# Kernel optimization log

Measured on AMD Instinct MI355X. Metric: run time of the kernel, lower is better.

The kernel has to match this reference:

```python
import jax, jax.numpy as jnp
import numpy as np

B, S, E, P = 4, 2048, 1024, 4096

def setup_inputs() -> dict:
    key = jax.random.key(0)
    kx, kk, kv = jax.random.split(key, 3)
    x = jax.random.normal(kx, (B, S, E), dtype=jnp.float32)
    K = jax.random.normal(kk, (P, E), dtype=jnp.float32)
    V = jax.random.normal(kv, (P, E), dtype=jnp.float32)
    return {"x": x, "K": K, "V": V}

def reference(x, K, V):
    # scores: [B, S, P] = x @ K^T scaled by 1/sqrt(E)
    scale = jnp.asarray(x.shape[-1], x.dtype) ** -0.5
    scores = jnp.einsum('bse,pe->bsp', x, K) * scale
    attn = jax.nn.softmax(scores, axis=-1)
    # output: [B, S, E] = attn @ V
    return jnp.einsum('bsp,pe->bse', attn, V)
```

## Files before the change

kernel.cpp:

```cpp
#include <hip/hip_runtime.h>
#include <hip/hip_bf16.h>

typedef __attribute__((ext_vector_type(8))) short bf16x8;
typedef __attribute__((ext_vector_type(4))) float f32x4;
typedef __attribute__((ext_vector_type(8))) unsigned short u16x8;

__device__ __forceinline__ unsigned short f2bf(float f) {
  union { float f; unsigned u; } c; c.f = f;
  unsigned u = c.u;
  u = (u + 0x7FFFu + ((u >> 16) & 1u)) >> 16;
  return (unsigned short)u;
}

__device__ __forceinline__ void gld_lds16(const void* g, void* l) {
  __builtin_amdgcn_global_load_lds(
      (__attribute__((address_space(1))) unsigned int*)g,
      (__attribute__((address_space(3))) unsigned int*)l,
      16, 0, 0);
}

__global__ void cvt_all(const float* __restrict__ x, unsigned short* __restrict__ x16,
                        const float* __restrict__ Kw, unsigned short* __restrict__ K16,
                        const float* __restrict__ V, unsigned short* __restrict__ Vt,
                        float* __restrict__ lsum) {
  const int b = blockIdx.x;
  if (b < 32) lsum[b * 256 + threadIdx.x] = 0.f;

  if (b < 6144) {
    const float* in;
    unsigned short* out;
    int i;
    if (b < 4096) {
      in = x; out = x16; i = (b * 256 + threadIdx.x) * 8;
    } else {
      in = Kw; out = K16; i = ((b - 4096) * 256 + threadIdx.x) * 8;
    }
    const float4* p = (const float4*)(in + i);
    float4 a = p[0], bb = p[1];
    u16x8 r;
    r[0] = f2bf(a.x); r[1] = f2bf(a.y); r[2] = f2bf(a.z); r[3] = f2bf(a.w);
    r[4] = f2bf(bb.x); r[5] = f2bf(bb.y); r[6] = f2bf(bb.z); r[7] = f2bf(bb.w);
    *(u16x8*)(out + i) = r;
  } else {
    __shared__ unsigned short t[64][65];
    const int tile = b - 6144;
    const int p0 = (tile & 63) * 64;
    const int e0 = (tile >> 6) * 64;
    const int tx = threadIdx.x & 63;
    const int ty = threadIdx.x >> 6;
#pragma unroll
    for (int i = 0; i < 16; ++i) {
      int p = ty + i * 4;
      t[p][tx] = f2bf(V[(size_t)(p0 + p) * 1024 + e0 + tx]);
    }
    __syncthreads();
#pragma unroll
    for (int i = 0; i < 16; ++i) {
      int e = ty + i * 4;
      Vt[(size_t)(e0 + e) * 4096 + p0 + tx] = t[tx][e];
    }
  }
}

template <int EPI>
__global__ __launch_bounds__(256) void gemm_nt(
    const unsigned short* __restrict__ A, const unsigned short* __restrict__ B,
    int M, int N, int Kd,
    unsigned short* __restrict__ Pout, float* __restrict__ lsum,
    float* __restrict__ Cout, const float* __restrict__ lin, float scale) {
  __shared__ __align__(16) unsigned short sA[128 * 64];
  __shared__ __align__(16) unsigned short sB[128 * 64];

  const int tid = threadIdx.x;
  const int lane = tid & 63;
  const int w = tid >> 6;
  const int wm = w >> 1;
  const int wn = w & 1;

  int row0, col0;
  if constexpr (EPI == 0) {
    row0 = blockIdx.y * 128;
    col0 = blockIdx.x * 128;
  } else {
    int bid = blockIdx.x;
    row0 = (((bid >> 6) << 3) | (bid & 7)) * 128;
    col0 = ((bid >> 3) & 7) * 128;
  }

  f32x4 acc[4][4] = {};

  const unsigned short* pA[4];
  const unsigned short* pB[4];
  char* ldsA[4];
  char* ldsB[4];
#pragma unroll
  for (int j = 0; j < 4; ++j) {
    int c = j * 256 + tid;
    int r = c >> 3;
    int cs = (c & 7) ^ (r & 7);
    pA[j] = A + (size_t)(row0 + r) * Kd + cs * 8;
    pB[j] = B + (size_t)(col0 + r) * Kd + cs * 8;
    int off = (j * 256 + (w << 6)) * 16;
    ldsA[j] = (char*)sA + off;
    ldsB[j] = (char*)sB + off;
  }

  const int q = lane >> 4;
  const int ml = lane & 15;
  const char* fA[2];
  const char* fB[2];
#pragma unroll
  for (int ks = 0; ks < 2; ++ks) {
    int cc = (ks * 4 + q) ^ (ml & 7);
    fA[ks] = (const char*)sA + (wm * 64 + ml) * 128 + cc * 16;
    fB[ks] = (const char*)sB + (wn * 64 + ml) * 128 + cc * 16;
  }

  const int kIters = Kd >> 6;
  for (int it = 0; it < kIters; ++it) {
    __syncthreads();
#pragma unroll
    for (int j = 0; j < 4; ++j) {
      gld_lds16(pA[j], ldsA[j]);
      gld_lds16(pB[j], ldsB[j]);
      pA[j] += 64;
      pB[j] += 64;
    }
    __syncthreads();

#pragma unroll
    for (int ks = 0; ks < 2; ++ks) {
      bf16x8 af[4], bfr[4];
#pragma unroll
      for (int mi = 0; mi < 4; ++mi) af[mi] = *(const bf16x8*)(fA[ks] + mi * 2048);
#pragma unroll
      for (int ni = 0; ni < 4; ++ni) bfr[ni] = *(const bf16x8*)(fB[ks] + ni * 2048);
#pragma unroll
      for (int mi = 0; mi < 4; ++mi)
#pragma unroll
        for (int ni = 0; ni < 4; ++ni)
          acc[mi][ni] = __builtin_amdgcn_mfma_f32_16x16x32_bf16(
              af[mi], bfr[ni], acc[mi][ni], 0, 0, 0);
    }
  }

  if constexpr (EPI == 0) {
#pragma unroll
    for (int mi = 0; mi < 4; ++mi) {
#pragma unroll
      for (int j = 0; j < 4; ++j) {
        int gr = row0 + wm * 64 + mi * 16 + q * 4 + j;
        float rsum = 0.f;
#pragma unroll
        for (int ni = 0; ni < 4; ++ni) {
          int gc = col0 + wn * 64 + ni * 16 + ml;
          float p = exp2f(acc[mi][ni][j] * scale);
          rsum += p;
          Pout[(size_t)gr * N + gc] = f2bf(p);
        }
        rsum += __shfl_xor(rsum, 1);
        rsum += __shfl_xor(rsum, 2);
        rsum += __shfl_xor(rsum, 4);
        rsum += __shfl_xor(rsum, 8);
        if (ml == 0) atomicAdd(&lsum[gr], rsum);
      }
    }
  } else {
#pragma unroll
    for (int mi = 0; mi < 4; ++mi) {
#pragma unroll
      for (int j = 0; j < 4; ++j) {
        int gr = row0 + wm * 64 + mi * 16 + q * 4 + j;
        float rl = 1.0f / lin[gr];
#pragma unroll
        for (int ni = 0; ni < 4; ++ni) {
          int gc = col0 + wn * 64 + ni * 16 + ml;
          Cout[(size_t)gr * N + gc] = acc[mi][ni][j] * rl;
        }
      }
    }
  }
}

extern "C" void kernel_launch(void* const* d_in, const int* in_sizes, int n_in,
                              void* d_out, int out_size, void* d_ws,
                              size_t ws_size, hipStream_t stream) {
  const float* x = (const float*)d_in[0];
  const float* Kw = (const float*)d_in[1];
  const float* Vw = (const float*)d_in[2];
  float* out = (float*)d_out;
  char* ws = (char*)d_ws;

  unsigned short* x16  = (unsigned short*)(ws);
  unsigned short* K16  = (unsigned short*)(ws + (16u << 20));
  unsigned short* V16t = (unsigned short*)(ws + (24u << 20));
  float*          lsum = (float*)(ws + (32u << 20));
  unsigned short* P16  = (unsigned short*)(ws + (33u << 20));

  cvt_all<<<7168, 256, 0, stream>>>(x, x16, Kw, K16, Vw, V16t, lsum);

  gemm_nt<0><<<dim3(32, 64), 256, 0, stream>>>(
      x16, K16, 8192, 4096, 1024, P16, lsum, nullptr, nullptr,
      0.03125f * 1.44269504088896340736f);
  gemm_nt<1><<<512, 256, 0, stream>>>(
      P16, V16t, 8192, 1024, 4096, nullptr, nullptr, out, lsum, 1.0f);
}
```

Baseline: 267.7 us.

## Rewrite both GEMMs as 8-wave double-buffered pipelined kernels with larger tiles

Replaces the 4-wave 128x128 single-buffered GEMM with a 512-thread kernel that uses 256x256 tiles for the score GEMM and 128x256 tiles for the PV GEMM. Global-to-LDS loads are double-buffered and issued in phases interleaved with MFMA blocks, with explicit waitcnt, barriers and setprio. It also adds an XCD-aware block remap. The aim is to hide load latency and raise data reuse per tile. The cost is more LDS per block, heavier register pressure, and a fragile hand-written synchronisation scheme.

```diff
diff --git a/kernel.cpp b/kernel.cpp
--- a/kernel.cpp
+++ b/kernel.cpp
@@ -63,100 +63,132 @@
 }
 
 template <int EPI>
-__global__ __launch_bounds__(256) void gemm_nt(
+__global__ __launch_bounds__(512, 2) void gemm8p(
     const unsigned short* __restrict__ A, const unsigned short* __restrict__ B,
-    int M, int N, int Kd,
     unsigned short* __restrict__ Pout, float* __restrict__ lsum,
     float* __restrict__ Cout, const float* __restrict__ lin, float scale) {
-  __shared__ __align__(16) unsigned short sA[128 * 64];
-  __shared__ __align__(16) unsigned short sB[128 * 64];
+  constexpr int BM = EPI ? 128 : 256;
+  constexpr int BN = 256;
+  constexpr int Kd = EPI ? 4096 : 1024;
+  constexpr int Nc = EPI ? 1024 : 4096;
+  constexpr int NT = Kd / 64;
+  constexpr int AU = BM / 128;
+  constexpr int NU = AU + 2;
+  constexpr int M_rep = BM / 32;
+  constexpr int PH = M_rep / 2;
+
+  __shared__ __align__(16) char lds[2 * NU * 16384];
 
   const int tid = threadIdx.x;
   const int lane = tid & 63;
   const int w = tid >> 6;
-  const int wm = w >> 1;
-  const int wn = w & 1;
-
-  int row0, col0;
-  if constexpr (EPI == 0) {
-    row0 = blockIdx.y * 128;
-    col0 = blockIdx.x * 128;
-  } else {
-    int bid = blockIdx.x;
-    row0 = (((bid >> 6) << 3) | (bid & 7)) * 128;
-    col0 = ((bid >> 3) & 7) * 128;
-  }
-
-  f32x4 acc[4][4] = {};
-
-  const unsigned short* pA[4];
-  const unsigned short* pB[4];
-  char* ldsA[4];
-  char* ldsB[4];
-#pragma unroll
-  for (int j = 0; j < 4; ++j) {
-    int c = j * 256 + tid;
-    int r = c >> 3;
-    int cs = (c & 7) ^ (r & 7);
-    pA[j] = A + (size_t)(row0 + r) * Kd + cs * 8;
-    pB[j] = B + (size_t)(col0 + r) * Kd + cs * 8;
-    int off = (j * 256 + (w << 6)) * 16;
-    ldsA[j] = (char*)sA + off;
-    ldsB[j] = (char*)sB + off;
-  }
-
+  const int wm = w >> 2;
+  const int wn = w & 3;
   const int q = lane >> 4;
   const int ml = lane & 15;
-  const char* fA[2];
-  const char* fB[2];
-#pragma unroll
-  for (int ks = 0; ks < 2; ++ks) {
-    int cc = (ks * 4 + q) ^ (ml & 7);
-    fA[ks] = (const char*)sA + (wm * 64 + ml) * 128 + cc * 16;
-    fB[ks] = (const char*)sB + (wn * 64 + ml) * 128 + cc * 16;
+
+  const int bid = blockIdx.x;
+  const int wg = (bid & 7) * (EPI ? 32 : 64) + (bid >> 3);
+  const int m_t = EPI ? (wg >> 2) : (wg >> 4);
+  const int n_t = EPI ? (wg & 3) : (wg & 15);
+  const int row0 = m_t * BM;
+  const int col0 = n_t * BN;
+
+  const int cr = tid >> 3;
+  const int ss = (tid & 7) ^ (cr & 7);
+  char* ldsw = lds + w * 1024 + lane * 16;
+
+  const int ccB = (q ^ (ml & 7)) * 16;
+  const int aOff = (EPI ? 0 : wm) * 16384 + ((EPI ? wm * 64 : 0) + ml) * 128 + ccB;
+  const int bOff = (AU + (wn >> 1)) * 16384 + ((wn & 1) * 64 + ml) * 128 + ccB;
+
+  f32x4 acc[M_rep][4] = {};
+  bf16x8 bF[4][2];
+
+  auto stA = [&](int a, int t, int buf) {
+    const unsigned short* s = A + (size_t)(row0 + a * 128 + cr) * Kd + t * 64 + ss * 8;
+    char* d = ldsw + (buf * NU + a) * 16384;
+    gld_lds16(s, d);
+    gld_lds16(s + (size_t)64 * Kd, d + 8192);
+  };
+  auto stB = [&](int b, int t, int buf) {
+    const unsigned short* s = B + (size_t)(col0 + b * 128 + cr) * Kd + t * 64 + ss * 8;
+    char* d = ldsw + (buf * NU + AU + b) * 16384;
+    gld_lds16(s, d);
+    gld_lds16(s + (size_t)64 * Kd, d + 8192);
+  };
+
+#pragma unroll
+  for (int a = 0; a < AU; ++a) stA(a, 0, 0);
+  stB(0, 0, 0); stB(1, 0, 0);
+  stB(0, 1, 1); stB(1, 1, 1);
+  asm volatile("s_waitcnt vmcnt(4)" ::: "memory");
+  __builtin_amdgcn_s_barrier();
+
+#pragma unroll 2
+  for (int g = 0; g < NT; ++g) {
+    const char* base = lds + (g & 1) * (NU * 16384);
+    const int tA = (g + 1) & (NT - 1);
+    const int bufA = (g + 1) & 1;
+    const int tB = (g + 2) & (NT - 1);
+    const int bufB = g & 1;
+#pragma unroll
+    for (int p = 0; p < PH; ++p) {
+      if (p == 0) {
+#pragma unroll
+        for (int ni = 0; ni < 4; ++ni)
+#pragma unroll
+          for (int ks = 0; ks < 2; ++ks)
+            bF[ni][ks] = *(const bf16x8*)(base + ((bOff ^ (ks * 64)) + ni * 2048));
+      }
+      bf16x8 aF[2][2];
+#pragma unroll
+      for (int i = 0; i < 2; ++i)
+#pragma unroll
+        for (int ks = 0; ks < 2; ++ks)
+          aF[i][ks] = *(const bf16x8*)(base + ((aOff ^ (ks * 64)) + (2 * p + i) * 2048));
+
+      if constexpr (EPI == 0) {
+        if (p == 0) stA(0, tA, bufA);
+        else if (p == 1) stA(1, tA, bufA);
+        else if (p == 2) stB(0, tB, bufB);
+        else stB(1, tB, bufB);
+      } else {
+        if (p == 0) stA(0, tA, bufA);
+        else { stB(0, tB, bufB); stB(1, tB, bufB); }
+      }
+
+      __builtin_amdgcn_s_barrier();
+      asm volatile("s_waitcnt lgkmcnt(0)" ::: "memory");
+      __builtin_amdgcn_sched_barrier(0);
+      __builtin_amdgcn_s_setprio(1);
+#pragma unroll
+      for (int ks = 0; ks < 2; ++ks)
+#pragma unroll
+        for (int i = 0; i < 2; ++i)
+#pragma unroll
+          for (int ni = 0; ni < 4; ++ni)
+            acc[2 * p + i][ni] = __builtin_amdgcn_mfma_f32_16x16x32_bf16(
+                aF[i][ks], bF[ni][ks], acc[2 * p + i][ni], 0, 0, 0);
+      __builtin_amdgcn_s_setprio(0);
+      if (p == PH - 1) asm volatile("s_waitcnt vmcnt(4)" ::: "memory");
+      __builtin_amdgcn_s_barrier();
+    }
   }
 
-  const int kIters = Kd >> 6;
-  for (int it = 0; it < kIters; ++it) {
-    __syncthreads();
-#pragma unroll
-    for (int j = 0; j < 4; ++j) {
-      gld_lds16(pA[j], ldsA[j]);
-      gld_lds16(pB[j], ldsB[j]);
-      pA[j] += 64;
-      pB[j] += 64;
-    }
-    __syncthreads();
-
-#pragma unroll
-    for (int ks = 0; ks < 2; ++ks) {
-      bf16x8 af[4], bfr[4];
-#pragma unroll
-      for (int mi = 0; mi < 4; ++mi) af[mi] = *(const bf16x8*)(fA[ks] + mi * 2048);
-#pragma unroll
-      for (int ni = 0; ni < 4; ++ni) bfr[ni] = *(const bf16x8*)(fB[ks] + ni * 2048);
-#pragma unroll
-      for (int mi = 0; mi < 4; ++mi)
-#pragma unroll
-        for (int ni = 0; ni < 4; ++ni)
-          acc[mi][ni] = __builtin_amdgcn_mfma_f32_16x16x32_bf16(
-              af[mi], bfr[ni], acc[mi][ni], 0, 0, 0);
-    }
-  }
-
   if constexpr (EPI == 0) {
 #pragma unroll
-    for (int mi = 0; mi < 4; ++mi) {
+    for (int mi = 0; mi < M_rep; ++mi) {
 #pragma unroll
       for (int j = 0; j < 4; ++j) {
-        int gr = row0 + wm * 64 + mi * 16 + q * 4 + j;
+        const int gr = row0 + wm * (BM / 2) + mi * 16 + q * 4 + j;
         float rsum = 0.f;
 #pragma unroll
         for (int ni = 0; ni < 4; ++ni) {
-          int gc = col0 + wn * 64 + ni * 16 + ml;
-          float p = exp2f(acc[mi][ni][j] * scale);
-          rsum += p;
-          Pout[(size_t)gr * N + gc] = f2bf(p);
+          const int gc = col0 + wn * 64 + ni * 16 + ml;
+          float pv = exp2f(acc[mi][ni][j] * scale);
+          rsum += pv;
+          Pout[(size_t)gr * Nc + gc] = f2bf(pv);
         }
         rsum += __shfl_xor(rsum, 1);
         rsum += __shfl_xor(rsum, 2);
@@ -167,15 +199,15 @@
     }
   } else {
 #pragma unroll
-    for (int mi = 0; mi < 4; ++mi) {
+    for (int mi = 0; mi < M_rep; ++mi) {
 #pragma unroll
       for (int j = 0; j < 4; ++j) {
-        int gr = row0 + wm * 64 + mi * 16 + q * 4 + j;
-        float rl = 1.0f / lin[gr];
+        const int gr = row0 + wm * (BM / 2) + mi * 16 + q * 4 + j;
+        const float rl = 1.0f / lin[gr];
 #pragma unroll
         for (int ni = 0; ni < 4; ++ni) {
-          int gc = col0 + wn * 64 + ni * 16 + ml;
-          Cout[(size_t)gr * N + gc] = acc[mi][ni][j] * rl;
+          const int gc = col0 + wn * 64 + ni * 16 + ml;
+          Cout[(size_t)gr * Nc + gc] = acc[mi][ni][j] * rl;
         }
       }
     }
@@ -199,9 +231,9 @@
 
   cvt_all<<<7168, 256, 0, stream>>>(x, x16, Kw, K16, Vw, V16t, lsum);
 
-  gemm_nt<0><<<dim3(32, 64), 256, 0, stream>>>(
-      x16, K16, 8192, 4096, 1024, P16, lsum, nullptr, nullptr,
+  gemm8p<0><<<512, 512, 0, stream>>>(
+      x16, K16, P16, lsum, nullptr, nullptr,
       0.03125f * 1.44269504088896340736f);
-  gemm_nt<1><<<512, 256, 0, stream>>>(
-      P16, V16t, 8192, 1024, 4096, nullptr, nullptr, out, lsum, 1.0f);
-}
+  gemm8p<1><<<256, 512, 0, stream>>>(
+      P16, V16t, nullptr, nullptr, out, lsum, 0.f);
+}
```

Result: faster. 255.7 us (-4.5%).

## Use 256x128 tiles with 32x32 MFMA and split-K for second GEMM

Applied to the files above, without the earlier changes.

Both GEMMs move from 128x128 tiles with 16x16x32 MFMA to 256x128 tiles using 32x32x16 MFMA, which gives more reuse per LDS load and fewer fragment reads. The second GEMM splits K in two and accumulates into the output with float atomics, so it runs 512 blocks of half depth; the output is zeroed in the conversion kernel. The V transpose now writes 16-byte vectors, and block indices are remapped for L2 locality. The cost is higher register and LDS use (launch_bounds 256,2) and extra atomic traffic on the output.

```diff
diff --git a/kernel.cpp b/kernel.cpp
--- a/kernel.cpp
+++ b/kernel.cpp
@@ -2,7 +2,7 @@
 #include <hip/hip_bf16.h>
 
 typedef __attribute__((ext_vector_type(8))) short bf16x8;
-typedef __attribute__((ext_vector_type(4))) float f32x4;
+typedef __attribute__((ext_vector_type(16))) float f32x16;
 typedef __attribute__((ext_vector_type(8))) unsigned short u16x8;
 
 __device__ __forceinline__ unsigned short f2bf(float f) {
@@ -22,18 +22,19 @@
 __global__ void cvt_all(const float* __restrict__ x, unsigned short* __restrict__ x16,
                         const float* __restrict__ Kw, unsigned short* __restrict__ K16,
                         const float* __restrict__ V, unsigned short* __restrict__ Vt,
-                        float* __restrict__ lsum) {
+                        float* __restrict__ lsum, float* __restrict__ outz) {
   const int b = blockIdx.x;
-  if (b < 32) lsum[b * 256 + threadIdx.x] = 0.f;
+  const int tid = threadIdx.x;
+  if (b < 32) lsum[b * 256 + tid] = 0.f;
 
   if (b < 6144) {
     const float* in;
     unsigned short* out;
     int i;
     if (b < 4096) {
-      in = x; out = x16; i = (b * 256 + threadIdx.x) * 8;
+      in = x; out = x16; i = (b * 256 + tid) * 8;
     } else {
-      in = Kw; out = K16; i = ((b - 4096) * 256 + threadIdx.x) * 8;
+      in = Kw; out = K16; i = ((b - 4096) * 256 + tid) * 8;
     }
     const float4* p = (const float4*)(in + i);
     float4 a = p[0], bb = p[1];
@@ -41,106 +42,109 @@
     r[0] = f2bf(a.x); r[1] = f2bf(a.y); r[2] = f2bf(a.z); r[3] = f2bf(a.w);
     r[4] = f2bf(bb.x); r[5] = f2bf(bb.y); r[6] = f2bf(bb.z); r[7] = f2bf(bb.w);
     *(u16x8*)(out + i) = r;
-  } else {
+  } else if (b < 7168) {
     __shared__ unsigned short t[64][65];
     const int tile = b - 6144;
     const int p0 = (tile & 63) * 64;
     const int e0 = (tile >> 6) * 64;
-    const int tx = threadIdx.x & 63;
-    const int ty = threadIdx.x >> 6;
+    const int tx = tid & 63;
+    const int ty = tid >> 6;
 #pragma unroll
     for (int i = 0; i < 16; ++i) {
       int p = ty + i * 4;
       t[p][tx] = f2bf(V[(size_t)(p0 + p) * 1024 + e0 + tx]);
     }
     __syncthreads();
-#pragma unroll
-    for (int i = 0; i < 16; ++i) {
-      int e = ty + i * 4;
-      Vt[(size_t)(e0 + e) * 4096 + p0 + tx] = t[tx][e];
-    }
+    const int op = (tid & 7) * 8;
+    const int oe = tid >> 3;
+#pragma unroll
+    for (int h = 0; h < 2; ++h) {
+      int e = oe + h * 32;
+      u16x8 r;
+#pragma unroll
+      for (int i = 0; i < 8; ++i) r[i] = t[op + i][e];
+      *(u16x8*)(Vt + (size_t)(e0 + e) * 4096 + p0 + op) = r;
+    }
+  } else {
+    size_t base = ((size_t)(b - 7168) * 256 + tid) * 16;
+    float4 z = {0.f, 0.f, 0.f, 0.f};
+#pragma unroll
+    for (int k = 0; k < 4; ++k) *(float4*)(outz + base + k * 4) = z;
   }
 }
 
 template <int EPI>
-__global__ __launch_bounds__(256) void gemm_nt(
+__global__ __launch_bounds__(256, 2) void gemm_tk(
     const unsigned short* __restrict__ A, const unsigned short* __restrict__ B,
-    int M, int N, int Kd,
     unsigned short* __restrict__ Pout, float* __restrict__ lsum,
     float* __restrict__ Cout, const float* __restrict__ lin, float scale) {
-  __shared__ __align__(16) unsigned short sA[128 * 64];
-  __shared__ __align__(16) unsigned short sB[128 * 64];
+  constexpr int Kd = EPI ? 4096 : 1024;
+  constexpr int Nc = EPI ? 1024 : 4096;
+  constexpr int KT = EPI ? 32 : 16;
+
+  __shared__ __align__(16) char lds[49152];
 
   const int tid = threadIdx.x;
   const int lane = tid & 63;
   const int w = tid >> 6;
   const int wm = w >> 1;
   const int wn = w & 1;
-
-  int row0, col0;
+  const int l31 = lane & 31;
+  const int q = lane >> 5;
+
+  int m_t, n_t, k0;
   if constexpr (EPI == 0) {
-    row0 = blockIdx.y * 128;
-    col0 = blockIdx.x * 128;
+    const int wg = (blockIdx.x & 7) * 128 + (blockIdx.x >> 3);
+    n_t = wg & 31; m_t = wg >> 5; k0 = 0;
   } else {
-    int bid = blockIdx.x;
-    row0 = (((bid >> 6) << 3) | (bid & 7)) * 128;
-    col0 = ((bid >> 3) & 7) * 128;
-  }
-
-  f32x4 acc[4][4] = {};
-
-  const unsigned short* pA[4];
-  const unsigned short* pB[4];
-  char* ldsA[4];
-  char* ldsB[4];
-#pragma unroll
-  for (int j = 0; j < 4; ++j) {
-    int c = j * 256 + tid;
-    int r = c >> 3;
-    int cs = (c & 7) ^ (r & 7);
-    pA[j] = A + (size_t)(row0 + r) * Kd + cs * 8;
-    pB[j] = B + (size_t)(col0 + r) * Kd + cs * 8;
-    int off = (j * 256 + (w << 6)) * 16;
-    ldsA[j] = (char*)sA + off;
-    ldsB[j] = (char*)sB + off;
-  }
-
-  const int q = lane >> 4;
-  const int ml = lane & 15;
-  const char* fA[2];
-  const char* fB[2];
-#pragma unroll
-  for (int ks = 0; ks < 2; ++ks) {
-    int cc = (ks * 4 + q) ^ (ml & 7);
-    fA[ks] = (const char*)sA + (wm * 64 + ml) * 128 + cc * 16;
-    fB[ks] = (const char*)sB + (wn * 64 + ml) * 128 + cc * 16;
-  }
-
-  const int kIters = Kd >> 6;
-  for (int it = 0; it < kIters; ++it) {
+    const int wg = (blockIdx.x & 7) * 64 + (blockIdx.x >> 3);
+    k0 = (wg & 1) * 2048; n_t = (wg >> 1) & 7; m_t = wg >> 4;
+  }
+  const int row0 = m_t * 256;
+  const int col0 = n_t * 128;
+
+  const int tr = tid >> 3;
+  const int ss = (tid & 7) ^ (tr & 7);
+  const unsigned short* pA = A + (size_t)(row0 + tr) * Kd + k0 + ss * 8;
+  const unsigned short* pB = B + (size_t)(col0 + tr) * Kd + k0 + ss * 8;
+  char* ldsAw = lds + w * 1024;
+  char* ldsBw = lds + 32768 + w * 1024;
+
+  const char* aBase = lds + (wm * 128 + l31) * 128;
+  const char* bBase = lds + 32768 + (wn * 64 + l31) * 128;
+  int ccx[4];
+#pragma unroll
+  for (int ks = 0; ks < 4; ++ks) ccx[ks] = ((ks * 2 + q) ^ (lane & 7)) * 16;
+
+  f32x16 acc[4][2] = {};
+
+  for (int t = 0; t < KT; ++t) {
     __syncthreads();
 #pragma unroll
-    for (int j = 0; j < 4; ++j) {
-      gld_lds16(pA[j], ldsA[j]);
-      gld_lds16(pB[j], ldsB[j]);
-      pA[j] += 64;
-      pB[j] += 64;
-    }
+    for (int i = 0; i < 8; ++i)
+      gld_lds16(pA + (size_t)i * 32 * Kd, ldsAw + i * 4096);
+#pragma unroll
+    for (int i = 0; i < 4; ++i)
+      gld_lds16(pB + (size_t)i * 32 * Kd, ldsBw + i * 4096);
+    pA += 64;
+    pB += 64;
     __syncthreads();
 
 #pragma unroll
-    for (int ks = 0; ks < 2; ++ks) {
-      bf16x8 af[4], bfr[4];
-#pragma unroll
-      for (int mi = 0; mi < 4; ++mi) af[mi] = *(const bf16x8*)(fA[ks] + mi * 2048);
-#pragma unroll
-      for (int ni = 0; ni < 4; ++ni) bfr[ni] = *(const bf16x8*)(fB[ks] + ni * 2048);
+    for (int ks = 0; ks < 4; ++ks) {
+      bf16x8 aF[4], bF[2];
 #pragma unroll
       for (int mi = 0; mi < 4; ++mi)
-#pragma unroll
-        for (int ni = 0; ni < 4; ++ni)
-          acc[mi][ni] = __builtin_amdgcn_mfma_f32_16x16x32_bf16(
-              af[mi], bfr[ni], acc[mi][ni], 0, 0, 0);
+        aF[mi] = *(const bf16x8*)(aBase + mi * 4096 + ccx[ks]);
+#pragma unroll
+      for (int ni = 0; ni < 2; ++ni)
+        bF[ni] = *(const bf16x8*)(bBase + ni * 4096 + ccx[ks]);
+#pragma unroll
+      for (int mi = 0; mi < 4; ++mi)
+#pragma unroll
+        for (int ni = 0; ni < 2; ++ni)
+          acc[mi][ni] = __builtin_amdgcn_mfma_f32_32x32x16_bf16(
+              aF[mi], bF[ni], acc[mi][ni], 0, 0, 0);
     }
   }
 
@@ -148,34 +152,35 @@
 #pragma unroll
     for (int mi = 0; mi < 4; ++mi) {
 #pragma unroll
-      for (int j = 0; j < 4; ++j) {
-        int gr = row0 + wm * 64 + mi * 16 + q * 4 + j;
+      for (int j = 0; j < 16; ++j) {
+        const int gr = row0 + wm * 128 + mi * 32 + (j & 3) + 8 * (j >> 2) + 4 * q;
         float rsum = 0.f;
 #pragma unroll
-        for (int ni = 0; ni < 4; ++ni) {
-          int gc = col0 + wn * 64 + ni * 16 + ml;
-          float p = exp2f(acc[mi][ni][j] * scale);
-          rsum += p;
-          Pout[(size_t)gr * N + gc] = f2bf(p);
+        for (int ni = 0; ni < 2; ++ni) {
+          const int gc = col0 + wn * 64 + ni * 32 + l31;
+          float pv = exp2f(acc[mi][ni][j] * scale);
+          rsum += pv;
+          Pout[(size_t)gr * Nc + gc] = f2bf(pv);
         }
         rsum += __shfl_xor(rsum, 1);
         rsum += __shfl_xor(rsum, 2);
         rsum += __shfl_xor(rsum, 4);
         rsum += __shfl_xor(rsum, 8);
-        if (ml == 0) atomicAdd(&lsum[gr], rsum);
+        rsum += __shfl_xor(rsum, 16);
+        if (l31 == 0) atomicAdd(&lsum[gr], rsum);
       }
     }
   } else {
 #pragma unroll
     for (int mi = 0; mi < 4; ++mi) {
 #pragma unroll
-      for (int j = 0; j < 4; ++j) {
-        int gr = row0 + wm * 64 + mi * 16 + q * 4 + j;
-        float rl = 1.0f / lin[gr];
-#pragma unroll
-        for (int ni = 0; ni < 4; ++ni) {
-          int gc = col0 + wn * 64 + ni * 16 + ml;
-          Cout[(size_t)gr * N + gc] = acc[mi][ni][j] * rl;
+      for (int j = 0; j < 16; ++j) {
+        const int gr = row0 + wm * 128 + mi * 32 + (j & 3) + 8 * (j >> 2) + 4 * q;
+        const float rl = 1.0f / lin[gr];
+#pragma unroll
+        for (int ni = 0; ni < 2; ++ni) {
+          const int gc = col0 + wn * 64 + ni * 32 + l31;
+          atomicAdd(&Cout[(size_t)gr * Nc + gc], acc[mi][ni][j] * rl);
         }
       }
     }
@@ -197,11 +202,11 @@
   float*          lsum = (float*)(ws + (32u << 20));
   unsigned short* P16  = (unsigned short*)(ws + (33u << 20));
 
-  cvt_all<<<7168, 256, 0, stream>>>(x, x16, Kw, K16, Vw, V16t, lsum);
-
-  gemm_nt<0><<<dim3(32, 64), 256, 0, stream>>>(
-      x16, K16, 8192, 4096, 1024, P16, lsum, nullptr, nullptr,
+  cvt_all<<<9216, 256, 0, stream>>>(x, x16, Kw, K16, Vw, V16t, lsum, out);
+
+  gemm_tk<0><<<1024, 256, 0, stream>>>(
+      x16, K16, P16, lsum, nullptr, nullptr,
       0.03125f * 1.44269504088896340736f);
-  gemm_nt<1><<<512, 256, 0, stream>>>(
-      P16, V16t, 8192, 1024, 4096, nullptr, nullptr, out, lsum, 1.0f);
-}
+  gemm_tk<1><<<512, 256, 0, stream>>>(
+      P16, V16t, nullptr, nullptr, out, lsum, 0.f);
+}
```

Result: slower. 341.7 us (+27.7%).
